# Optimization experiments

Hardware: AMD Instinct MI355X
Metric: run time of the kernel (lower is better)

Reference implementation:

```python
import jax, jax.numpy as jnp
import numpy as np

B, C = 16384, 2048
DELTA_REL = 0.1


def setup_inputs() -> dict:
    key = jax.random.key(0)
    k1, k2, k3 = jax.random.split(key, 3)
    logits = jax.random.normal(k1, (B, C), dtype=jnp.float32)
    u = jax.random.uniform(k2, (B, C), dtype=jnp.float32)
    lab = (jax.random.uniform(k3, (B, C)) > 0.7).astype(jnp.float32)
    targets = jnp.where(u < 0.4, jnp.float32(jnp.nan), lab)
    return {"logits": logits, "targets": targets, "epoch": 3}


def _large_loss_rejection(logits, targets, epoch):
    unknown = jnp.isnan(targets)
    # unknown_to_negative: NaN -> 0 (negative label)
    t = jnp.where(unknown, 0.0, targets)
    # stable BCE-with-logits: softplus(x) - x*t
    losses = jax.nn.softplus(logits) - logits * t

    # --- no-grad mask construction ---
    ul = jax.lax.stop_gradient(losses) * unknown.astype(losses.dtype)
    percent = jnp.minimum(epoch * DELTA_REL, 1.0).astype(jnp.float32)
    n_unknown = jnp.count_nonzero(ul)
    k = jnp.round(n_unknown.astype(jnp.float32) * percent).astype(jnp.int32)
    k = jnp.maximum(k, 1)
    # k-th largest value of flattened unknown losses = topk(k).values.min()
    sorted_desc = jnp.sort(ul.reshape(-1))[::-1]
    loss_threshold = jax.lax.dynamic_slice(sorted_desc, (k - 1,), (1,))[0]
    lambdas = jnp.where(ul > loss_threshold, 0.0, 1.0)

    return losses * lambdas  # reduction='none'


def reference(logits, targets, epoch):
    return _large_loss_rejection(logits, targets, epoch)
```

## Files before the change

kernel.cpp:

```cpp
#include <hip/hip_runtime.h>
#include <math.h>

typedef float    f32x4 __attribute__((ext_vector_type(4)));
typedef unsigned u32x4 __attribute__((ext_vector_type(4)));

#define HBIG_OFF   0u
#define H12_OFF    16384u
#define H64_OFF    20480u
#define SH12_OFF   20544u
#define SHSUB_OFF  24640u
#define CTRL_OFF   24840u
#define FINE_OFF   24864u
#define ZERO_WORDS 25376u
#define GRAY_OFF   25376u
#define GRAY_CAP   440000u
#define EB_OFF     (GRAY_OFF + GRAY_CAP)
#define CAND_OFF   25376u
#define CAND_CAP   880000u
#define LBUF       2048u
#define DELTA_S    2500LL
#define VMARGIN    16384u

#define FLOOR_BITS 0x36000000u


__device__ __forceinline__ float softplus_exact(float x) {
    float ax = fabsf(x);
    float e = (float)exp(-(double)ax);
    float l = (float)log1p((double)e);
    return fmaxf(x, 0.0f) + l;
}
__device__ __forceinline__ unsigned exact_bits(float x) {
    return __float_as_uint(softplus_exact(x));
}

__device__ __forceinline__ unsigned refine_core(float x, float ax, float e,
                                                float sp) {
    unsigned cb = __float_as_uint(sp);
    float mf = 64.0f + 8.0f * ax;
    if (x < 0.0f) mf += __builtin_amdgcn_rcpf(e);
    bool need = (cb < FLOOR_BITS) || (mf >= 524288.0f);
    if (!need) {
        unsigned m = (unsigned)mf;
        unsigned low = cb & 0xFFFFFu;
        need = (low < m) || (low >= 0x100000u - m);
    }
    if (need) cb = exact_bits(x);
    return cb;
}
__device__ __forceinline__ unsigned refine_A(float x) {
    float ax = fabsf(x);
    float e = __expf(-ax);
    float sp = fmaxf(x, 0.0f) + __logf(1.0f + e);
    return refine_core(x, ax, e, sp);
}
__device__ __forceinline__ unsigned known_loss_bits(float x, float t) {
    float ax = fabsf(x);
    float e = __expf(-ax);
    float sp = fmaxf(x, 0.0f) + __logf(1.0f + e);
    return __float_as_uint(sp - x * t);
}

__global__ __launch_bounds__(256) void k0a_shist(
    const float* __restrict__ lg, const float* __restrict__ tg,
    unsigned* __restrict__ ws, long long n) {
    __shared__ unsigned sh[4096];
    for (int i = threadIdx.x; i < 4096; i += 256) sh[i] = 0;
    __syncthreads();
    long long units = n >> 9;
    long long u = (long long)blockIdx.x * 256 + threadIdx.x;
    if (u < units) {
        const f32x4* lg4 = (const f32x4*)lg;
        const f32x4* tg4 = (const f32x4*)tg;
        long long b = u * 128;
        f32x4 xa = lg4[b], xb = lg4[b + 1];
        f32x4 ta = tg4[b], tb = tg4[b + 1];
        float xs[8] = {xa.x, xa.y, xa.z, xa.w, xb.x, xb.y, xb.z, xb.w};
        float ts[8] = {ta.x, ta.y, ta.z, ta.w, tb.x, tb.y, tb.z, tb.w};
#pragma unroll
        for (int c = 0; c < 8; ++c)
            if (isnan(ts[c])) {
                unsigned cb = refine_A(xs[c]);
                if (cb) atomicAdd(&sh[cb >> 20], 1u);
            }
    }
    __syncthreads();
    for (int i = threadIdx.x; i < 4096; i += 256)
        if (sh[i]) atomicAdd(&ws[SH12_OFF + i], sh[i]);
}

__global__ __launch_bounds__(256) void k0b_sbin(
    unsigned* __restrict__ ws, const int* __restrict__ epoch_ptr) {
    const unsigned* sh12 = ws + SH12_OFF;
    unsigned* ctrl = ws + CTRL_OFF;
    __shared__ unsigned long long chunk[256];
    int t = threadIdx.x;
    unsigned long long s = 0;
    for (int j = 0; j < 16; ++j) s += sh12[t * 16 + j];
    chunk[t] = s;
    __syncthreads();
    if (t == 0) {
        unsigned long long tot = 0;
        for (int c = 0; c < 256; ++c) tot += chunk[c];
        if (tot == 0) {
            ctrl[7] = 1u;
            ctrl[8] = 0u; ctrl[9] = 0u; ctrl[19] = 0u;
            ctrl[17] = 0u; ctrl[18] = 0u;
            return;
        }
        int epoch = epoch_ptr[0];
        float percent = fminf((float)epoch * 0.1f, 1.0f);
        long long ks = (long long)((double)percent * (double)tot + 0.5);
        if (ks < 1) ks = 1;
        if (ks > (long long)tot) ks = (long long)tot;
        long long cum = 0;
        int bE = 0;
        for (int c = 255; c >= 0; --c) {
            if (cum + (long long)chunk[c] >= ks) {
                long long cc = cum;
                for (int j = 15; j >= 0; --j) {
                    unsigned v = sh12[c * 16 + j];
                    if (cc + (long long)v >= ks) { bE = c * 16 + j; break; }
                    cc += v;
                }
                break;
            }
            cum += chunk[c];
        }
        ctrl[13] = (unsigned)bE;
        ctrl[17] = (bE > 0) ? (unsigned)(bE - 1) : 0u;
        ctrl[18] = (bE < 4095) ? (unsigned)(bE + 1) : 4095u;
        ctrl[19] = (unsigned)ks;
    }
}

__global__ __launch_bounds__(256) void k0c_ssub(
    const float* __restrict__ lg, const float* __restrict__ tg,
    unsigned* __restrict__ ws, long long n) {
    if (ws[CTRL_OFF + 7] != 0u) return;
    unsigned lob = ws[CTRL_OFF + 17], hib = ws[CTRL_OFF + 18];
    unsigned rlo = lob << 20, rhi = (hib + 1u) << 20;
    __shared__ unsigned sh[192];
    if (threadIdx.x < 192) sh[threadIdx.x] = 0;
    __syncthreads();
    long long units = n >> 9;
    long long u = (long long)blockIdx.x * 256 + threadIdx.x;
    if (u < units) {
        const f32x4* lg4 = (const f32x4*)lg;
        const f32x4* tg4 = (const f32x4*)tg;
        long long b = u * 128;
        f32x4 xa = lg4[b], xb = lg4[b + 1];
        f32x4 ta = tg4[b], tb = tg4[b + 1];
        float xs[8] = {xa.x, xa.y, xa.z, xa.w, xb.x, xb.y, xb.z, xb.w};
        float ts[8] = {ta.x, ta.y, ta.z, ta.w, tb.x, tb.y, tb.z, tb.w};
#pragma unroll
        for (int c = 0; c < 8; ++c)
            if (isnan(ts[c])) {
                unsigned cb = refine_A(xs[c]);
                if (cb >= rlo && cb < rhi && (hib < 4095u || cb >= rlo))
                    atomicAdd(&sh[(cb - rlo) >> 14], 1u);
            }
    }
    __syncthreads();
    if (threadIdx.x < 192 && sh[threadIdx.x])
        atomicAdd(&ws[SHSUB_OFF + threadIdx.x], sh[threadIdx.x]);
}

__global__ __launch_bounds__(256) void k0d_window(unsigned* __restrict__ ws) {
    unsigned* ctrl = ws + CTRL_OFF;
    if (ctrl[7] != 0u) return;
    __shared__ unsigned long long red[256];
    __shared__ unsigned arr[192];
    int t = threadIdx.x;
    unsigned hib = ctrl[18];
    unsigned long long s = 0;
    for (int b = t; b < 4096; b += 256)
        if ((unsigned)b > hib) s += ws[SH12_OFF + b];
    red[t] = s;
    if (t < 192) arr[t] = ws[SHSUB_OFF + t];
    __syncthreads();
    for (int off = 128; off > 0; off >>= 1) {
        if (t < off) red[t] += red[t + off];
        __syncthreads();
    }
    if (t == 0) {
        unsigned lob = ctrl[17];
        unsigned base = lob << 20;
        int nsub = (int)(hib - lob + 1u) * 64;
        long long ks = (long long)ctrl[19];
        long long lo_t = ks - DELTA_S;
        long long hi_t = ks + DELTA_S;
        long long cum = (long long)red[0];
        unsigned est_hi = base + ((unsigned)nsub << 14);
        unsigned est_lo = base;
        bool fh = false, fl = false;
        for (int j = nsub - 1; j >= 0; --j) {
            if (!fh && cum + (long long)arr[j] > lo_t) {
                est_hi = base + ((unsigned)(j + 1) << 14);
                fh = true;
            }
            cum += arr[j];
            if (!fl && cum >= hi_t) {
                est_lo = base + ((unsigned)j << 14);
                fl = true;
            }
            if (fh && fl) break;
        }
        if (!fh) est_hi = base;
        ctrl[8] = est_lo;
        ctrl[9] = est_hi;
    }
}

__device__ __forceinline__ unsigned kA_elem(float x, float t, unsigned idx,
                                            unsigned* __restrict__ shh,
                                            unsigned* __restrict__ sha,
                                            unsigned* __restrict__ buf,
                                            unsigned* __restrict__ lcnt,
                                            unsigned elo, unsigned ehi) {
    float ax = fabsf(x);
    float e = __expf(-ax);
    float sp = fmaxf(x, 0.0f) + __logf(1.0f + e);
    if (isnan(t)) {
        unsigned cb = refine_core(x, ax, e, sp);
        if (cb != 0u) atomicAdd(&shh[cb >> 20], 1u);
        if (cb >= ehi) { atomicAdd(sha, 1u); return 0u; }
        if (cb >= elo) {
            unsigned li = atomicAdd(lcnt, 1u);
            if (li < LBUF) buf[li] = idx;
        }
        return cb;
    }
    return __float_as_uint(sp - x * t);
}

__global__ __launch_bounds__(256) void kA_main(
    const float* __restrict__ lg, const float* __restrict__ tg,
    float* __restrict__ out, unsigned* __restrict__ ws, long long n) {
    __shared__ unsigned shh[4096];
    __shared__ unsigned buf[LBUF];
    __shared__ unsigned lcnt, sha, gbase;
    for (int i = threadIdx.x; i < 4096; i += 256) shh[i] = 0;
    if (threadIdx.x == 0) { lcnt = 0; sha = 0; }
    __syncthreads();
    unsigned elo = ws[CTRL_OFF + 8], ehi = ws[CTRL_OFF + 9];

    long long n8 = n >> 3;
    long long tid = (long long)blockIdx.x * 256 + threadIdx.x;
    long long stride = (long long)gridDim.x * 256;
    const f32x4* lg4 = (const f32x4*)lg;
    const f32x4* tg4 = (const f32x4*)tg;
    f32x4* out4 = (f32x4*)out;

    long long i = tid;
    f32x4 xa, xb, ta, tb;
    if (i < n8) {
        xa = lg4[2 * i]; xb = lg4[2 * i + 1];
        ta = __builtin_nontemporal_load(&tg4[2 * i]);
        tb = __builtin_nontemporal_load(&tg4[2 * i + 1]);
    }
    while (i < n8) {
        long long j = i + stride;
        f32x4 nxa, nxb, nta, ntb;
        if (j < n8) {
            nxa = lg4[2 * j]; nxb = lg4[2 * j + 1];
            nta = __builtin_nontemporal_load(&tg4[2 * j]);
            ntb = __builtin_nontemporal_load(&tg4[2 * j + 1]);
        }
        unsigned base = (unsigned)(i * 8);
        f32x4 oa, ob_;
        oa.x = __uint_as_float(kA_elem(xa.x, ta.x, base + 0, shh, &sha, buf, &lcnt, elo, ehi));
        oa.y = __uint_as_float(kA_elem(xa.y, ta.y, base + 1, shh, &sha, buf, &lcnt, elo, ehi));
        oa.z = __uint_as_float(kA_elem(xa.z, ta.z, base + 2, shh, &sha, buf, &lcnt, elo, ehi));
        oa.w = __uint_as_float(kA_elem(xa.w, ta.w, base + 3, shh, &sha, buf, &lcnt, elo, ehi));
        ob_.x = __uint_as_float(kA_elem(xb.x, tb.x, base + 4, shh, &sha, buf, &lcnt, elo, ehi));
        ob_.y = __uint_as_float(kA_elem(xb.y, tb.y, base + 5, shh, &sha, buf, &lcnt, elo, ehi));
        ob_.z = __uint_as_float(kA_elem(xb.z, tb.z, base + 6, shh, &sha, buf, &lcnt, elo, ehi));
        ob_.w = __uint_as_float(kA_elem(xb.w, tb.w, base + 7, shh, &sha, buf, &lcnt, elo, ehi));
        out4[2 * i] = oa;
        out4[2 * i + 1] = ob_;
        xa = nxa; xb = nxb; ta = nta; tb = ntb;
        i = j;
    }
    if (tid == 0) {
        for (long long q = (n >> 3) << 3; q < n; ++q)
            out[q] = __uint_as_float(
                kA_elem(lg[q], tg[q], (unsigned)q, shh, &sha, buf, &lcnt, elo, ehi));
    }
    __syncthreads();
    for (int q = threadIdx.x; q < 4096; q += 256)
        if (shh[q]) atomicAdd(&ws[H12_OFF + q], shh[q]);
    if (threadIdx.x == 0) {
        if (sha) atomicAdd(&ws[CTRL_OFF + 11], sha);
        unsigned add = (lcnt > LBUF) ? (GRAY_CAP + 1u) : lcnt;
        gbase = atomicAdd(&ws[CTRL_OFF + 10], add);
    }
    __syncthreads();
    unsigned c2 = lcnt < LBUF ? lcnt : LBUF;
    for (unsigned q = threadIdx.x; q < c2; q += 256) {
        unsigned gi = gbase + q;
        if (gi < GRAY_CAP) ws[GRAY_OFF + gi] = buf[q];
    }
}

__global__ __launch_bounds__(256) void k2_route(
    unsigned* __restrict__ ws, const int* __restrict__ epoch_ptr) {
    const unsigned* hist12 = ws + H12_OFF;
    unsigned* ctrl = ws + CTRL_OFF;
    __shared__ unsigned long long chunk[256];
    int t = threadIdx.x;
    unsigned long long s = 0;
    for (int j = 0; j < 16; ++j) s += hist12[t * 16 + j];
    chunk[t] = s;
    __syncthreads();
    if (t == 0) {
        unsigned long long tot = 0;
        for (int c = 0; c < 256; ++c) tot += chunk[c];
        int epoch = epoch_ptr[0];
        float percent = fminf((float)epoch * 0.1f, 1.0f);
        float nf = (float)tot;
        float kr = rintf(nf * percent);
        long long k = (long long)kr;
        if (k < 1) k = 1;
        long long cum = 0;
        int b = -1;
        long long kprime = 0;
        for (int c = 255; c >= 0; --c) {
            if (cum + (long long)chunk[c] >= k) {
                long long cc = cum;
                for (int j = 15; j >= 0; --j) {
                    unsigned v = hist12[c * 16 + j];
                    if (cc + (long long)v >= k) {
                        b = c * 16 + j; kprime = k - cc; break;
                    }
                    cc += v;
                }
                break;
            }
            cum += chunk[c];
        }
        ctrl[0] = (unsigned)b;
        ctrl[1] = (unsigned)kprime;
        if (b < 0) {
            ctrl[2] = 0u;
            ctrl[4] = 0xFFFFFFFFu;
            ctrl[6] = 0u;
            ctrl[7] = 2u;
            return;
        }
        unsigned lo12 = (unsigned)b << 20;
        double vlo = (double)__uint_as_float(lo12);
        double vhi = (double)__uint_as_float(lo12 + 0xFFFFFu);
        double mb = 1e9;
        if (vlo > 1e-30) {
            double xlo = vlo + log1p(-exp(-vlo)) - 0.001;
            double xhi = vhi + log1p(-exp(-vhi)) + 0.001;
            double axmax = fmax(fabs(xlo), fabs(xhi));
            mb = 64.0 + 8.0 * ceil(axmax);
            if (xlo < 0.0) mb += exp(fmin(-xlo, 30.0));
            mb *= 2.0;
        }
        ctrl[6] = (mb >= 8192.0) ? 8192u : (unsigned)mb;
        unsigned f = ctrl[7];
        unsigned g = ctrl[10], a = ctrl[11];
        unsigned elo = ctrl[8], ehi = ctrl[9];
        long long rank = k - (long long)a;
        if (g > GRAY_CAP || rank < 1 || rank > (long long)g ||
            ehi < elo + 2u * VMARGIN)
            f = 1u;
        else {
            ctrl[12] = (unsigned)rank;
            unsigned W = ehi - elo;
            unsigned sft = 0;
            while (((unsigned long long)16384u << sft) < (unsigned long long)W)
                ++sft;
            ctrl[15] = sft;
        }
        ctrl[7] = f;
    }
}

__global__ __launch_bounds__(256) void G1_exact(
    const float* __restrict__ lg, unsigned* __restrict__ ws) {
    if (ws[CTRL_OFF + 7] != 0u) return;
    unsigned gcount = ws[CTRL_OFF + 10];
    unsigned elo = ws[CTRL_OFF + 8], ehi = ws[CTRL_OFF + 9];
    unsigned sft = ws[CTRL_OFF + 15];
    long long tid = (long long)blockIdx.x * 256 + threadIdx.x;
    long long stride = (long long)gridDim.x * 256;
    for (long long g = tid; g < (long long)gcount; g += stride) {
        unsigned idx = ws[GRAY_OFF + g];
        unsigned eb = exact_bits(lg[idx]);
        ws[EB_OFF + g] = eb;
        unsigned bin = (eb < elo) ? 0u
                     : (eb >= ehi) ? 16383u : ((eb - elo) >> sft);
        if (bin > 16383u) bin = 16383u;
        atomicAdd(&ws[HBIG_OFF + bin], 1u);
    }
}

__global__ __launch_bounds__(1024) void G2a_selbin(unsigned* __restrict__ ws) {
    unsigned* ctrl = ws + CTRL_OFF;
    if (ctrl[7] != 0u) return;
    __shared__ unsigned long long csum[1024];
    int t = threadIdx.x;
    unsigned long long s = 0;
    for (int j = 0; j < 16; ++j) s += ws[HBIG_OFF + t * 16 + j];
    csum[t] = s;
    __syncthreads();
    if (t == 0) {
        long long rank = (long long)ctrl[12];
        long long cum = 0;
        int sel = -1;
        long long rem = 1;
        for (int c = 1023; c >= 0; --c) {
            if (cum + (long long)csum[c] >= rank) {
                long long cc = cum;
                for (int j = 15; j >= 0; --j) {
                    unsigned v = ws[HBIG_OFF + c * 16 + j];
                    if (cc + (long long)v >= rank) {
                        sel = c * 16 + j; rem = rank - cc; break;
                    }
                    cc += v;
                }
                break;
            }
            cum += csum[c];
        }
        if (sel < 0) { ctrl[7] = 1u; return; }
        ctrl[14] = (unsigned)sel;
        ctrl[16] = (unsigned)rem;
    }
}

__global__ __launch_bounds__(256) void G2b_fine(unsigned* __restrict__ ws) {
    if (ws[CTRL_OFF + 7] != 0u) return;
    unsigned gcount = ws[CTRL_OFF + 10];
    unsigned elo = ws[CTRL_OFF + 8], ehi = ws[CTRL_OFF + 9];
    unsigned sft = ws[CTRL_OFF + 15];
    unsigned bsel = ws[CTRL_OFF + 14];
    long long tid = (long long)blockIdx.x * 256 + threadIdx.x;
    long long stride = (long long)gridDim.x * 256;
    for (long long g = tid; g < (long long)gcount; g += stride) {
        unsigned eb = ws[EB_OFF + g];
        if (eb >= elo && eb < ehi) {
            unsigned off = eb - elo;
            if ((off >> sft) == bsel)
                atomicAdd(&ws[FINE_OFF + (off - (bsel << sft))], 1u);
        }
    }
}

__global__ __launch_bounds__(512) void G2c_thr(unsigned* __restrict__ ws) {
    unsigned* ctrl = ws + CTRL_OFF;
    if (ctrl[7] != 0u) return;
    __shared__ unsigned fine[512];
    int t = threadIdx.x;
    unsigned sft = ctrl[15];
    unsigned binw = 1u << sft;
    if (binw > 512u) { if (t == 0) ctrl[7] = 1u; return; }
    if ((unsigned)t < binw) fine[t] = ws[FINE_OFF + t];
    __syncthreads();
    if (t == 0) {
        unsigned elo = ctrl[8], ehi = ctrl[9];
        unsigned binlo = elo + (ctrl[14] << sft);
        long long rem = (long long)ctrl[16];
        long long cum = 0;
        bool found = false;
        unsigned thr = 0;
        for (int o = (int)binw - 1; o >= 0; --o) {
            cum += fine[o];
            if (cum >= rem) { thr = binlo + (unsigned)o; found = true; break; }
        }
        if (!found || thr < elo + VMARGIN || thr > ehi - VMARGIN)
            ctrl[7] = 1u;
        else
            ctrl[2] = thr;
    }
}

__global__ __launch_bounds__(256) void kD_fix(
    unsigned* __restrict__ ob, const unsigned* __restrict__ ws) {
    if (ws[CTRL_OFF + 7] != 0u) return;
    unsigned gcount = ws[CTRL_OFF + 10];
    unsigned thr = ws[CTRL_OFF + 2];
    long long tid = (long long)blockIdx.x * 256 + threadIdx.x;
    long long stride = (long long)gridDim.x * 256;
    for (long long g = tid; g < (long long)gcount; g += stride) {
        if (ws[EB_OFF + g] > thr) ob[ws[GRAY_OFF + g]] = 0u;
    }
}

__global__ __launch_bounds__(256) void fkB(
    const float* __restrict__ lg, const float* __restrict__ tg,
    unsigned* __restrict__ ws, long long n) {
    if (ws[CTRL_OFF + 7] != 1u) return;
    unsigned b12 = ws[CTRL_OFF + 0];
    if (b12 == 0xFFFFFFFFu) return;
    unsigned lo12 = b12 << 20, hi12 = lo12 + (1u << 20);
    unsigned m = ws[CTRL_OFF + 6];
    __shared__ unsigned sh[64];
    __shared__ float buf[LBUF];
    __shared__ unsigned lcnt, gbase;
    if (threadIdx.x < 64) sh[threadIdx.x] = 0;
    if (threadIdx.x == 0) lcnt = 0;
    __syncthreads();
    float* cand = (float*)(ws + CAND_OFF);
    unsigned* cnt = ws + CTRL_OFF + 3;
    long long n4 = n >> 2;
    long long tid = (long long)blockIdx.x * 256 + threadIdx.x;
    long long stride = (long long)gridDim.x * 256;
    const f32x4* lg4 = (const f32x4*)lg;
    const f32x4* tg4 = (const f32x4*)tg;
    for (long long i = tid; i < n4; i += stride) {
        f32x4 x4 = lg4[i], t4 = tg4[i];
        float xs[4] = {x4.x, x4.y, x4.z, x4.w};
        float ts[4] = {t4.x, t4.y, t4.z, t4.w};
#pragma unroll
        for (int c = 0; c < 4; ++c) {
            if (isnan(ts[c])) {
                float x = xs[c];
                unsigned cb = refine_A(x);
                if (cb >= lo12 && cb < hi12) {
                    unsigned d = cb & 16383u;
                    unsigned rB = (d < m || d >= 16384u - m) ? exact_bits(x) : cb;
                    atomicAdd(&sh[(rB >> 14) & 63u], 1u);
                    unsigned li = atomicAdd(&lcnt, 1u);
                    if (li < LBUF) buf[li] = x;
                }
            }
        }
    }
    if (tid == 0) {
        for (long long q = (n4 << 2); q < n; ++q) {
            if (isnan(tg[q])) {
                float x = lg[q];
                unsigned cb = refine_A(x);
                if (cb >= lo12 && cb < hi12) {
                    unsigned d = cb & 16383u;
                    unsigned rB = (d < m || d >= 16384u - m) ? exact_bits(x) : cb;
                    atomicAdd(&sh[(rB >> 14) & 63u], 1u);
                    unsigned idx = atomicAdd(cnt, 1u);
                    if (idx < CAND_CAP) cand[idx] = x;
                }
            }
        }
    }
    __syncthreads();
    if (threadIdx.x < 64 && sh[threadIdx.x])
        atomicAdd(&ws[H64_OFF + threadIdx.x], sh[threadIdx.x]);
    if (threadIdx.x == 0) {
        unsigned add = (lcnt > LBUF) ? (CAND_CAP + 1u) : lcnt;
        gbase = atomicAdd(cnt, add);
    }
    __syncthreads();
    unsigned c2 = lcnt < LBUF ? lcnt : LBUF;
    for (unsigned q = threadIdx.x; q < c2; q += 256) {
        unsigned gi = gbase + q;
        if (gi < CAND_CAP) cand[gi] = buf[q];
    }
}

__global__ void fk4(unsigned* __restrict__ ws) {
    unsigned* ctrl = ws + CTRL_OFF;
    if (ctrl[7] != 1u) return;
    if (ctrl[0] == 0xFFFFFFFFu) return;
    if (threadIdx.x == 0) {
        long long kprime = (long long)ctrl[1];
        long long cum = 0;
        int s = 0;
        long long kpp = 1;
        for (int j = 63; j >= 0; --j) {
            unsigned v = ws[H64_OFF + j];
            if (cum + (long long)v >= kprime) { s = j; kpp = kprime - cum; break; }
            cum += v;
        }
        ctrl[4] = (ctrl[0] << 20) + ((unsigned)s << 14);
        ctrl[5] = (unsigned)kpp;
    }
}

__global__ __launch_bounds__(256) void fkC(
    const float* __restrict__ lg, const float* __restrict__ tg,
    unsigned* __restrict__ ws, long long n) {
    if (ws[CTRL_OFF + 7] != 1u) return;
    unsigned wlo = ws[CTRL_OFF + 4];
    if (wlo == 0xFFFFFFFFu) return;
    unsigned whi = wlo + 16384u;
    unsigned m = ws[CTRL_OFF + 6];
    unsigned b12 = ws[CTRL_OFF + 0];
    unsigned lo12 = b12 << 20, hi12 = lo12 + (1u << 20);
    unsigned glo = (wlo - lo12 > m) ? wlo - m : lo12;
    unsigned ghi = (hi12 - whi > m) ? whi + m : hi12;
    unsigned count = ws[CTRL_OFF + 3];
    long long tid = (long long)blockIdx.x * 256 + threadIdx.x;
    long long stride = (long long)gridDim.x * 256;
    if (count <= CAND_CAP) {
        const float* cand = (const float*)(ws + CAND_OFF);
        for (long long i = tid; i < (long long)count; i += stride) {
            float x = cand[i];
            unsigned u = refine_A(x);
            if (u >= glo && u < ghi) {
                unsigned eb = exact_bits(x);
                unsigned d = u & 16383u;
                unsigned rB = (d < m || d >= 16384u - m) ? eb : u;
                if (rB >= wlo && rB < whi) {
                    unsigned off = eb - wlo;
                    if (off < 16384u) atomicAdd(&ws[HBIG_OFF + off], 1u);
                }
            }
        }
    } else {
        for (long long q = tid; q < n; q += stride) {
            if (isnan(tg[q])) {
                float x = lg[q];
                unsigned u = refine_A(x);
                if (u >= glo && u < ghi) {
                    unsigned eb = exact_bits(x);
                    unsigned d = u & 16383u;
                    unsigned rB = (d < m || d >= 16384u - m) ? eb : u;
                    if (rB >= wlo && rB < whi) {
                        unsigned off = eb - wlo;
                        if (off < 16384u) atomicAdd(&ws[HBIG_OFF + off], 1u);
                    }
                }
            }
        }
    }
}

__global__ __launch_bounds__(1024) void fk6(unsigned* __restrict__ ws) {
    unsigned* ctrl = ws + CTRL_OFF;
    if (ctrl[7] != 1u) return;
    if (ctrl[4] == 0xFFFFFFFFu) return;
    __shared__ unsigned long long csum[1024];
    int t = threadIdx.x;
    unsigned long long s = 0;
    for (int j = 0; j < 16; ++j) s += ws[HBIG_OFF + t * 16 + j];
    csum[t] = s;
    __syncthreads();
    if (t == 0) {
        long long kpp = (long long)ctrl[5];
        long long cum = 0;
        int sel = 0;
        long long rem = kpp;
        for (int c = 1023; c >= 0; --c) {
            if (cum + (long long)csum[c] >= kpp) { sel = c; rem = kpp - cum; break; }
            cum += csum[c];
        }
        long long cc = 0;
        int bsel = 0;
        for (int j = 15; j >= 0; --j) {
            unsigned v = ws[HBIG_OFF + sel * 16 + j];
            if (cc + (long long)v >= rem) { bsel = j; break; }
            cc += v;
        }
        ctrl[2] = ctrl[4] + (unsigned)(sel * 16 + bsel);
    }
}

__global__ __launch_bounds__(256) void fkD(
    const float* __restrict__ lg, const float* __restrict__ tg,
    float* __restrict__ out, const unsigned* __restrict__ ws, long long n) {
    if (ws[CTRL_OFF + 7] != 1u) return;
    unsigned thr = ws[CTRL_OFF + 2];
    unsigned m = ws[CTRL_OFF + 6];
    long long n4 = n >> 2;
    long long tid = (long long)blockIdx.x * 256 + threadIdx.x;
    long long stride = (long long)gridDim.x * 256;
    const f32x4* lg4 = (const f32x4*)lg;
    const f32x4* tg4 = (const f32x4*)tg;
    f32x4* out4 = (f32x4*)out;
    for (long long i = tid; i < n4; i += stride) {
        f32x4 x4 = lg4[i], t4 = tg4[i];
        float xs[4] = {x4.x, x4.y, x4.z, x4.w};
        float ts[4] = {t4.x, t4.y, t4.z, t4.w};
        f32x4 o;
        float os[4];
#pragma unroll
        for (int c = 0; c < 4; ++c) {
            float x = xs[c], t = ts[c];
            if (isnan(t)) {
                unsigned cb = refine_A(x);
                unsigned udiff = (cb > thr) ? cb - thr : thr - cb;
                unsigned r;
                if (udiff <= m) {
                    unsigned eb = exact_bits(x);
                    r = (eb > thr) ? 0u : eb;
                } else {
                    r = (cb > thr) ? 0u : cb;
                }
                os[c] = __uint_as_float(r);
            } else {
                os[c] = __uint_as_float(known_loss_bits(x, t));
            }
        }
        o.x = os[0]; o.y = os[1]; o.z = os[2]; o.w = os[3];
        out4[i] = o;
    }
    if (tid == 0) {
        for (long long q = (n4 << 2); q < n; ++q) {
            float x = lg[q], t = tg[q];
            if (isnan(t)) {
                unsigned cb = refine_A(x);
                unsigned udiff = (cb > thr) ? cb - thr : thr - cb;
                unsigned eb, r;
                if (udiff <= m) { eb = exact_bits(x); r = (eb > thr) ? 0u : eb; }
                else r = (cb > thr) ? 0u : cb;
                out[q] = __uint_as_float(r);
            } else {
                out[q] = __uint_as_float(known_loss_bits(x, t));
            }
        }
    }
}

extern "C" void kernel_launch(void* const* d_in, const int* in_sizes, int n_in,
                              void* d_out, int out_size, void* d_ws, size_t ws_size,
                              hipStream_t stream) {
    const float* lg = (const float*)d_in[0];
    const float* tg = (const float*)d_in[1];
    const int* epoch = (const int*)d_in[2];
    float* out = (float*)d_out;
    unsigned* ob = (unsigned*)d_out;
    unsigned* ws = (unsigned*)d_ws;
    long long n = (long long)in_sizes[0];

    (void)hipMemsetAsync(d_ws, 0, (size_t)ZERO_WORDS * 4, stream);

    k0a_shist<<<256, 256, 0, stream>>>(lg, tg, ws, n);
    k0b_sbin<<<1, 256, 0, stream>>>(ws, epoch);
    k0c_ssub<<<256, 256, 0, stream>>>(lg, tg, ws, n);
    k0d_window<<<1, 256, 0, stream>>>(ws);
    kA_main<<<2048, 256, 0, stream>>>(lg, tg, out, ws, n);
    k2_route<<<1, 256, 0, stream>>>(ws, epoch);
    G1_exact<<<128, 256, 0, stream>>>(lg, ws);
    G2a_selbin<<<1, 1024, 0, stream>>>(ws);
    G2b_fine<<<128, 256, 0, stream>>>(ws);
    G2c_thr<<<1, 512, 0, stream>>>(ws);
    kD_fix<<<128, 256, 0, stream>>>(ob, ws);
    fkB<<<2048, 256, 0, stream>>>(lg, tg, ws, n);
    fk4<<<1, 64, 0, stream>>>(ws);
    fkC<<<1024, 256, 0, stream>>>(lg, tg, ws, n);
    fk6<<<1, 1024, 0, stream>>>(ws);
    fkD<<<2048, 256, 0, stream>>>(lg, tg, out, ws, n);
}
```

Measured before the change: 266.7 us.

## Drop per-element histogram in main pass, stash gray-zone logits, defer histogram to fallback

```diff
diff --git a/kernel.cpp b/kernel.cpp
--- a/kernel.cpp
+++ b/kernel.cpp
@@ -13,7 +13,7 @@
 #define FINE_OFF   24864u
 #define ZERO_WORDS 25376u
 #define GRAY_OFF   25376u
-#define GRAY_CAP   440000u
+#define GRAY_CAP   450000u
 #define EB_OFF     (GRAY_OFF + GRAY_CAP)
 #define CAND_OFF   25376u
 #define CAND_CAP   880000u
@@ -213,21 +213,21 @@
 }
 
 __device__ __forceinline__ unsigned kA_elem(float x, float t, unsigned idx,
-                                            unsigned* __restrict__ shh,
-                                            unsigned* __restrict__ sha,
-                                            unsigned* __restrict__ buf,
-                                            unsigned* __restrict__ lcnt,
-                                            unsigned elo, unsigned ehi) {
+                                            unsigned elo, unsigned ehi,
+                                            unsigned& nz, unsigned& ab,
+                                            unsigned* __restrict__ bufi,
+                                            unsigned* __restrict__ bufx,
+                                            unsigned* __restrict__ lcnt) {
     float ax = fabsf(x);
     float e = __expf(-ax);
     float sp = fmaxf(x, 0.0f) + __logf(1.0f + e);
     if (isnan(t)) {
         unsigned cb = refine_core(x, ax, e, sp);
-        if (cb != 0u) atomicAdd(&shh[cb >> 20], 1u);
-        if (cb >= ehi) { atomicAdd(sha, 1u); return 0u; }
+        nz += (cb != 0u) ? 1u : 0u;
+        if (cb >= ehi) { ++ab; return 0u; }
         if (cb >= elo) {
             unsigned li = atomicAdd(lcnt, 1u);
-            if (li < LBUF) buf[li] = idx;
+            if (li < LBUF) { bufi[li] = idx; bufx[li] = __float_as_uint(x); }
         }
         return cb;
     }
@@ -237,13 +237,15 @@
 __global__ __launch_bounds__(256) void kA_main(
     const float* __restrict__ lg, const float* __restrict__ tg,
     float* __restrict__ out, unsigned* __restrict__ ws, long long n) {
-    __shared__ unsigned shh[4096];
-    __shared__ unsigned buf[LBUF];
-    __shared__ unsigned lcnt, sha, gbase;
-    for (int i = threadIdx.x; i < 4096; i += 256) shh[i] = 0;
-    if (threadIdx.x == 0) { lcnt = 0; sha = 0; }
-    __syncthreads();
+    __shared__ unsigned bufi[LBUF];
+    __shared__ unsigned bufx[LBUF];
+    __shared__ unsigned lcnt, gbase, snz, sab;
+    if (threadIdx.x == 0) { lcnt = 0; snz = 0; sab = 0; }
+    __syncthreads();
+    unsigned flag = ws[CTRL_OFF + 7];
     unsigned elo = ws[CTRL_OFF + 8], ehi = ws[CTRL_OFF + 9];
+    if (flag != 0u) { elo = 0xFFFFFFFFu; ehi = 0xFFFFFFFFu; }
+    unsigned nz = 0, ab = 0;
 
     long long n8 = n >> 3;
     long long tid = (long long)blockIdx.x * 256 + threadIdx.x;
@@ -252,46 +254,74 @@
     const f32x4* tg4 = (const f32x4*)tg;
     f32x4* out4 = (f32x4*)out;
 
-    long long i = tid;
-    f32x4 xa, xb, ta, tb;
-    if (i < n8) {
-        xa = lg4[2 * i]; xb = lg4[2 * i + 1];
-        ta = __builtin_nontemporal_load(&tg4[2 * i]);
-        tb = __builtin_nontemporal_load(&tg4[2 * i + 1]);
-    }
-    while (i < n8) {
-        long long j = i + stride;
-        f32x4 nxa, nxb, nta, ntb;
-        if (j < n8) {
-            nxa = lg4[2 * j]; nxb = lg4[2 * j + 1];
-            nta = __builtin_nontemporal_load(&tg4[2 * j]);
-            ntb = __builtin_nontemporal_load(&tg4[2 * j + 1]);
-        }
-        unsigned base = (unsigned)(i * 8);
-        f32x4 oa, ob_;
-        oa.x = __uint_as_float(kA_elem(xa.x, ta.x, base + 0, shh, &sha, buf, &lcnt, elo, ehi));
-        oa.y = __uint_as_float(kA_elem(xa.y, ta.y, base + 1, shh, &sha, buf, &lcnt, elo, ehi));
-        oa.z = __uint_as_float(kA_elem(xa.z, ta.z, base + 2, shh, &sha, buf, &lcnt, elo, ehi));
-        oa.w = __uint_as_float(kA_elem(xa.w, ta.w, base + 3, shh, &sha, buf, &lcnt, elo, ehi));
-        ob_.x = __uint_as_float(kA_elem(xb.x, tb.x, base + 4, shh, &sha, buf, &lcnt, elo, ehi));
-        ob_.y = __uint_as_float(kA_elem(xb.y, tb.y, base + 5, shh, &sha, buf, &lcnt, elo, ehi));
-        ob_.z = __uint_as_float(kA_elem(xb.z, tb.z, base + 6, shh, &sha, buf, &lcnt, elo, ehi));
-        ob_.w = __uint_as_float(kA_elem(xb.w, tb.w, base + 7, shh, &sha, buf, &lcnt, elo, ehi));
-        out4[2 * i] = oa;
-        out4[2 * i + 1] = ob_;
-        xa = nxa; xb = nxb; ta = nta; tb = ntb;
-        i = j;
+    if (n8 % stride == 0) {
+        long long iters = n8 / stride;
+        f32x4 xa0, xb0, ta0, tb0, xa1, xb1, ta1, tb1;
+        {
+            long long i = tid;
+            xa0 = lg4[2 * i]; xb0 = lg4[2 * i + 1];
+            ta0 = __builtin_nontemporal_load(&tg4[2 * i]);
+            tb0 = __builtin_nontemporal_load(&tg4[2 * i + 1]);
+        }
+        if (iters > 1) {
+            long long i = tid + stride;
+            xa1 = lg4[2 * i]; xb1 = lg4[2 * i + 1];
+            ta1 = __builtin_nontemporal_load(&tg4[2 * i]);
+            tb1 = __builtin_nontemporal_load(&tg4[2 * i + 1]);
+        }
+        for (long long it = 0; it < iters; ++it) {
+            f32x4 pa, pb, pta, ptb;
+            if (it + 2 < iters) {
+                long long i = tid + (it + 2) * stride;
+                pa = lg4[2 * i]; pb = lg4[2 * i + 1];
+                pta = __builtin_nontemporal_load(&tg4[2 * i]);
+                ptb = __builtin_nontemporal_load(&tg4[2 * i + 1]);
+            }
+            long long i = tid + it * stride;
+            unsigned base = (unsigned)(i * 8);
+            f32x4 oa, ob_;
+            oa.x = __uint_as_float(kA_elem(xa0.x, ta0.x, base + 0, elo, ehi, nz, ab, bufi, bufx, &lcnt));
+            oa.y = __uint_as_float(kA_elem(xa0.y, ta0.y, base + 1, elo, ehi, nz, ab, bufi, bufx, &lcnt));
+            oa.z = __uint_as_float(kA_elem(xa0.z, ta0.z, base + 2, elo, ehi, nz, ab, bufi, bufx, &lcnt));
+            oa.w = __uint_as_float(kA_elem(xa0.w, ta0.w, base + 3, elo, ehi, nz, ab, bufi, bufx, &lcnt));
+            ob_.x = __uint_as_float(kA_elem(xb0.x, tb0.x, base + 4, elo, ehi, nz, ab, bufi, bufx, &lcnt));
+            ob_.y = __uint_as_float(kA_elem(xb0.y, tb0.y, base + 5, elo, ehi, nz, ab, bufi, bufx, &lcnt));
+            ob_.z = __uint_as_float(kA_elem(xb0.z, tb0.z, base + 6, elo, ehi, nz, ab, bufi, bufx, &lcnt));
+            ob_.w = __uint_as_float(kA_elem(xb0.w, tb0.w, base + 7, elo, ehi, nz, ab, bufi, bufx, &lcnt));
+            out4[2 * i] = oa;
+            out4[2 * i + 1] = ob_;
+            xa0 = xa1; xb0 = xb1; ta0 = ta1; tb0 = tb1;
+            xa1 = pa; xb1 = pb; ta1 = pta; tb1 = ptb;
+        }
+    } else {
+        for (long long i = tid; i < n8; i += stride) {
+            f32x4 xa = lg4[2 * i], xb = lg4[2 * i + 1];
+            f32x4 ta = tg4[2 * i], tb = tg4[2 * i + 1];
+            unsigned base = (unsigned)(i * 8);
+            f32x4 oa, ob_;
+            oa.x = __uint_as_float(kA_elem(xa.x, ta.x, base + 0, elo, ehi, nz, ab, bufi, bufx, &lcnt));
+            oa.y = __uint_as_float(kA_elem(xa.y, ta.y, base + 1, elo, ehi, nz, ab, bufi, bufx, &lcnt));
+            oa.z = __uint_as_float(kA_elem(xa.z, ta.z, base + 2, elo, ehi, nz, ab, bufi, bufx, &lcnt));
+            oa.w = __uint_as_float(kA_elem(xa.w, ta.w, base + 3, elo, ehi, nz, ab, bufi, bufx, &lcnt));
+            ob_.x = __uint_as_float(kA_elem(xb.x, tb.x, base + 4, elo, ehi, nz, ab, bufi, bufx, &lcnt));
+            ob_.y = __uint_as_float(kA_elem(xb.y, tb.y, base + 5, elo, ehi, nz, ab, bufi, bufx, &lcnt));
+            ob_.z = __uint_as_float(kA_elem(xb.z, tb.z, base + 6, elo, ehi, nz, ab, bufi, bufx, &lcnt));
+            ob_.w = __uint_as_float(kA_elem(xb.w, tb.w, base + 7, elo, ehi, nz, ab, bufi, bufx, &lcnt));
+            out4[2 * i] = oa;
+            out4[2 * i + 1] = ob_;
+        }
     }
     if (tid == 0) {
         for (long long q = (n >> 3) << 3; q < n; ++q)
             out[q] = __uint_as_float(
-                kA_elem(lg[q], tg[q], (unsigned)q, shh, &sha, buf, &lcnt, elo, ehi));
-    }
-    __syncthreads();
-    for (int q = threadIdx.x; q < 4096; q += 256)
-        if (shh[q]) atomicAdd(&ws[H12_OFF + q], shh[q]);
+                kA_elem(lg[q], tg[q], (unsigned)q, elo, ehi, nz, ab, bufi, bufx, &lcnt));
+    }
+    if (nz) atomicAdd(&snz, nz);
+    if (ab) atomicAdd(&sab, ab);
+    __syncthreads();
     if (threadIdx.x == 0) {
-        if (sha) atomicAdd(&ws[CTRL_OFF + 11], sha);
+        if (snz) atomicAdd(&ws[CTRL_OFF + 20], snz);
+        if (sab) atomicAdd(&ws[CTRL_OFF + 11], sab);
         unsigned add = (lcnt > LBUF) ? (GRAY_CAP + 1u) : lcnt;
         gbase = atomicAdd(&ws[CTRL_OFF + 10], add);
     }
@@ -299,14 +329,192 @@
     unsigned c2 = lcnt < LBUF ? lcnt : LBUF;
     for (unsigned q = threadIdx.x; q < c2; q += 256) {
         unsigned gi = gbase + q;
-        if (gi < GRAY_CAP) ws[GRAY_OFF + gi] = buf[q];
-    }
-}
-
-__global__ __launch_bounds__(256) void k2_route(
+        if (gi < GRAY_CAP) {
+            ws[GRAY_OFF + gi] = bufi[q];
+            ws[EB_OFF + gi] = bufx[q];
+        }
+    }
+}
+
+__global__ void k2_route(unsigned* __restrict__ ws,
+                         const int* __restrict__ epoch_ptr) {
+    if (threadIdx.x != 0) return;
+    unsigned* ctrl = ws + CTRL_OFF;
+    unsigned tot = ctrl[20];
+    int epoch = epoch_ptr[0];
+    float percent = fminf((float)epoch * 0.1f, 1.0f);
+    float nf = (float)tot;
+    float kr = rintf(nf * percent);
+    long long k = (long long)kr;
+    if (k < 1) k = 1;
+    if (tot == 0u) { ctrl[2] = 0u; ctrl[7] = 2u; return; }
+    if (ctrl[7] != 0u) return;
+    unsigned g = ctrl[10], a = ctrl[11];
+    unsigned elo = ctrl[8], ehi = ctrl[9];
+    long long rank = k - (long long)a;
+    if (g > GRAY_CAP || rank < 1 || rank > (long long)g ||
+        ehi < elo + 2u * VMARGIN) {
+        ctrl[7] = 1u;
+        return;
+    }
+    ctrl[12] = (unsigned)rank;
+    unsigned W = ehi - elo;
+    unsigned sft = 0;
+    while (((unsigned long long)16384u << sft) < (unsigned long long)W) ++sft;
+    ctrl[15] = sft;
+}
+
+__global__ __launch_bounds__(256) void G1_exact(unsigned* __restrict__ ws) {
+    if (ws[CTRL_OFF + 7] != 0u) return;
+    unsigned gcount = ws[CTRL_OFF + 10];
+    unsigned elo = ws[CTRL_OFF + 8], ehi = ws[CTRL_OFF + 9];
+    unsigned sft = ws[CTRL_OFF + 15];
+    long long tid = (long long)blockIdx.x * 256 + threadIdx.x;
+    long long stride = (long long)gridDim.x * 256;
+    for (long long g = tid; g < (long long)gcount; g += stride) {
+        float x = __uint_as_float(ws[EB_OFF + g]);
+        unsigned eb = exact_bits(x);
+        ws[EB_OFF + g] = eb;
+        unsigned bin = (eb < elo) ? 0u
+                     : (eb >= ehi) ? 16383u : ((eb - elo) >> sft);
+        if (bin > 16383u) bin = 16383u;
+        atomicAdd(&ws[HBIG_OFF + bin], 1u);
+    }
+}
+
+__global__ __launch_bounds__(1024) void G2a_selbin(unsigned* __restrict__ ws) {
+    unsigned* ctrl = ws + CTRL_OFF;
+    if (ctrl[7] != 0u) return;
+    __shared__ unsigned long long csum[1024];
+    int t = threadIdx.x;
+    unsigned long long s = 0;
+    for (int j = 0; j < 16; ++j) s += ws[HBIG_OFF + t * 16 + j];
+    csum[t] = s;
+    __syncthreads();
+    if (t == 0) {
+        long long rank = (long long)ctrl[12];
+        long long cum = 0;
+        int sel = -1;
+        long long rem = 1;
+        for (int c = 1023; c >= 0; --c) {
+            if (cum + (long long)csum[c] >= rank) {
+                long long cc = cum;
+                for (int j = 15; j >= 0; --j) {
+                    unsigned v = ws[HBIG_OFF + c * 16 + j];
+                    if (cc + (long long)v >= rank) {
+                        sel = c * 16 + j; rem = rank - cc; break;
+                    }
+                    cc += v;
+                }
+                break;
+            }
+            cum += csum[c];
+        }
+        if (sel < 0) { ctrl[7] = 1u; return; }
+        ctrl[14] = (unsigned)sel;
+        ctrl[16] = (unsigned)rem;
+    }
+}
+
+__global__ __launch_bounds__(256) void G2b_fine(unsigned* __restrict__ ws) {
+    if (ws[CTRL_OFF + 7] != 0u) return;
+    unsigned gcount = ws[CTRL_OFF + 10];
+    unsigned elo = ws[CTRL_OFF + 8], ehi = ws[CTRL_OFF + 9];
+    unsigned sft = ws[CTRL_OFF + 15];
+    unsigned bsel = ws[CTRL_OFF + 14];
+    long long tid = (long long)blockIdx.x * 256 + threadIdx.x;
+    long long stride = (long long)gridDim.x * 256;
+    for (long long g = tid; g < (long long)gcount; g += stride) {
+        unsigned eb = ws[EB_OFF + g];
+        if (eb >= elo && eb < ehi) {
+            unsigned off = eb - elo;
+            if ((off >> sft) == bsel)
+                atomicAdd(&ws[FINE_OFF + (off - (bsel << sft))], 1u);
+        }
+    }
+}
+
+__global__ __launch_bounds__(512) void G2c_thr(unsigned* __restrict__ ws) {
+    unsigned* ctrl = ws + CTRL_OFF;
+    if (ctrl[7] != 0u) return;
+    __shared__ unsigned fine[512];
+    int t = threadIdx.x;
+    unsigned sft = ctrl[15];
+    unsigned binw = 1u << sft;
+    if (binw > 512u) { if (t == 0) ctrl[7] = 1u; return; }
+    if ((unsigned)t < binw) fine[t] = ws[FINE_OFF + t];
+    __syncthreads();
+    if (t == 0) {
+        unsigned elo = ctrl[8], ehi = ctrl[9];
+        unsigned binlo = elo + (ctrl[14] << sft);
+        long long rem = (long long)ctrl[16];
+        long long cum = 0;
+        bool found = false;
+        unsigned thr = 0;
+        for (int o = (int)binw - 1; o >= 0; --o) {
+            cum += fine[o];
+            if (cum >= rem) { thr = binlo + (unsigned)o; found = true; break; }
+        }
+        if (!found || thr < elo + VMARGIN || thr > ehi - VMARGIN)
+            ctrl[7] = 1u;
+        else
+            ctrl[2] = thr;
+    }
+}
+
+__global__ __launch_bounds__(256) void kD_fix(
+    unsigned* __restrict__ ob, const unsigned* __restrict__ ws) {
+    if (ws[CTRL_OFF + 7] != 0u) return;
+    unsigned gcount = ws[CTRL_OFF + 10];
+    unsigned thr = ws[CTRL_OFF + 2];
+    long long tid = (long long)blockIdx.x * 256 + threadIdx.x;
+    long long stride = (long long)gridDim.x * 256;
+    for (long long g = tid; g < (long long)gcount; g += stride) {
+        if (ws[EB_OFF + g] > thr) ob[ws[GRAY_OFF + g]] = 0u;
+    }
+}
+
+__global__ __launch_bounds__(256) void fkA_hist(
+    const float* __restrict__ lg, const float* __restrict__ tg,
+    unsigned* __restrict__ ws, long long n) {
+    if (ws[CTRL_OFF + 7] != 1u) return;
+    __shared__ unsigned sh[4096];
+    for (int i = threadIdx.x; i < 4096; i += 256) sh[i] = 0;
+    __syncthreads();
+    long long n4 = n >> 2;
+    long long tid = (long long)blockIdx.x * 256 + threadIdx.x;
+    long long stride = (long long)gridDim.x * 256;
+    const f32x4* lg4 = (const f32x4*)lg;
+    const f32x4* tg4 = (const f32x4*)tg;
+    for (long long i = tid; i < n4; i += stride) {
+        f32x4 x4 = lg4[i], t4 = tg4[i];
+        float xs[4] = {x4.x, x4.y, x4.z, x4.w};
+        float ts[4] = {t4.x, t4.y, t4.z, t4.w};
+#pragma unroll
+        for (int c = 0; c < 4; ++c)
+            if (isnan(ts[c])) {
+                unsigned cb = refine_A(xs[c]);
+                if (cb) atomicAdd(&sh[cb >> 20], 1u);
+            }
+    }
+    if (tid == 0) {
+        for (long long q = (n4 << 2); q < n; ++q)
+            if (isnan(tg[q])) {
+                unsigned cb = refine_A(lg[q]);
+                if (cb) atomicAdd(&sh[cb >> 20], 1u);
+            }
+    }
+    __syncthreads();
+    for (int i = threadIdx.x; i < 4096; i += 256)
+        if (sh[i]) atomicAdd(&ws[H12_OFF + i], sh[i]);
+}
+
+__global__ __launch_bounds__(256) void fk2_sel(
     unsigned* __restrict__ ws, const int* __restrict__ epoch_ptr) {
+    unsigned* ctrl = ws + CTRL_OFF;
+    if (ctrl[7] != 1u) return;
+    for (unsigned i = threadIdx.x; i < 16384u; i += 256) ws[HBIG_OFF + i] = 0;
     const unsigned* hist12 = ws + H12_OFF;
-    unsigned* ctrl = ws + CTRL_OFF;
     __shared__ unsigned long long chunk[256];
     int t = threadIdx.x;
     unsigned long long s = 0;
@@ -316,6 +524,7 @@
     if (t == 0) {
         unsigned long long tot = 0;
         for (int c = 0; c < 256; ++c) tot += chunk[c];
+        if (tot == 0) { ctrl[2] = 0u; ctrl[7] = 2u; return; }
         int epoch = epoch_ptr[0];
         float percent = fminf((float)epoch * 0.1f, 1.0f);
         float nf = (float)tot;
@@ -341,13 +550,6 @@
         }
         ctrl[0] = (unsigned)b;
         ctrl[1] = (unsigned)kprime;
-        if (b < 0) {
-            ctrl[2] = 0u;
-            ctrl[4] = 0xFFFFFFFFu;
-            ctrl[6] = 0u;
-            ctrl[7] = 2u;
-            return;
-        }
         unsigned lo12 = (unsigned)b << 20;
         double vlo = (double)__uint_as_float(lo12);
         double vhi = (double)__uint_as_float(lo12 + 0xFFFFFu);
@@ -361,133 +563,6 @@
             mb *= 2.0;
         }
         ctrl[6] = (mb >= 8192.0) ? 8192u : (unsigned)mb;
-        unsigned f = ctrl[7];
-        unsigned g = ctrl[10], a = ctrl[11];
-        unsigned elo = ctrl[8], ehi = ctrl[9];
-        long long rank = k - (long long)a;
-        if (g > GRAY_CAP || rank < 1 || rank > (long long)g ||
-            ehi < elo + 2u * VMARGIN)
-            f = 1u;
-        else {
-            ctrl[12] = (unsigned)rank;
-            unsigned W = ehi - elo;
-            unsigned sft = 0;
-            while (((unsigned long long)16384u << sft) < (unsigned long long)W)
-                ++sft;
-            ctrl[15] = sft;
-        }
-        ctrl[7] = f;
-    }
-}
-
-__global__ __launch_bounds__(256) void G1_exact(
-    const float* __restrict__ lg, unsigned* __restrict__ ws) {
-    if (ws[CTRL_OFF + 7] != 0u) return;
-    unsigned gcount = ws[CTRL_OFF + 10];
-    unsigned elo = ws[CTRL_OFF + 8], ehi = ws[CTRL_OFF + 9];
-    unsigned sft = ws[CTRL_OFF + 15];
-    long long tid = (long long)blockIdx.x * 256 + threadIdx.x;
-    long long stride = (long long)gridDim.x * 256;
-    for (long long g = tid; g < (long long)gcount; g += stride) {
-        unsigned idx = ws[GRAY_OFF + g];
-        unsigned eb = exact_bits(lg[idx]);
-        ws[EB_OFF + g] = eb;
-        unsigned bin = (eb < elo) ? 0u
-                     : (eb >= ehi) ? 16383u : ((eb - elo) >> sft);
-        if (bin > 16383u) bin = 16383u;
-        atomicAdd(&ws[HBIG_OFF + bin], 1u);
-    }
-}
-
-__global__ __launch_bounds__(1024) void G2a_selbin(unsigned* __restrict__ ws) {
-    unsigned* ctrl = ws + CTRL_OFF;
-    if (ctrl[7] != 0u) return;
-    __shared__ unsigned long long csum[1024];
-    int t = threadIdx.x;
-    unsigned long long s = 0;
-    for (int j = 0; j < 16; ++j) s += ws[HBIG_OFF + t * 16 + j];
-    csum[t] = s;
-    __syncthreads();
-    if (t == 0) {
-        long long rank = (long long)ctrl[12];
-        long long cum = 0;
-        int sel = -1;
-        long long rem = 1;
-        for (int c = 1023; c >= 0; --c) {
-            if (cum + (long long)csum[c] >= rank) {
-                long long cc = cum;
-                for (int j = 15; j >= 0; --j) {
-                    unsigned v = ws[HBIG_OFF + c * 16 + j];
-                    if (cc + (long long)v >= rank) {
-                        sel = c * 16 + j; rem = rank - cc; break;
-                    }
-                    cc += v;
-                }
-                break;
-            }
-            cum += csum[c];
-        }
-        if (sel < 0) { ctrl[7] = 1u; return; }
-        ctrl[14] = (unsigned)sel;
-        ctrl[16] = (unsigned)rem;
-    }
-}
-
-__global__ __launch_bounds__(256) void G2b_fine(unsigned* __restrict__ ws) {
-    if (ws[CTRL_OFF + 7] != 0u) return;
-    unsigned gcount = ws[CTRL_OFF + 10];
-    unsigned elo = ws[CTRL_OFF + 8], ehi = ws[CTRL_OFF + 9];
-    unsigned sft = ws[CTRL_OFF + 15];
-    unsigned bsel = ws[CTRL_OFF + 14];
-    long long tid = (long long)blockIdx.x * 256 + threadIdx.x;
-    long long stride = (long long)gridDim.x * 256;
-    for (long long g = tid; g < (long long)gcount; g += stride) {
-        unsigned eb = ws[EB_OFF + g];
-        if (eb >= elo && eb < ehi) {
-            unsigned off = eb - elo;
-            if ((off >> sft) == bsel)
-                atomicAdd(&ws[FINE_OFF + (off - (bsel << sft))], 1u);
-        }
-    }
-}
-
-__global__ __launch_bounds__(512) void G2c_thr(unsigned* __restrict__ ws) {
-    unsigned* ctrl = ws + CTRL_OFF;
-    if (ctrl[7] != 0u) return;
-    __shared__ unsigned fine[512];
-    int t = threadIdx.x;
-    unsigned sft = ctrl[15];
-    unsigned binw = 1u << sft;
-    if (binw > 512u) { if (t == 0) ctrl[7] = 1u; return; }
-    if ((unsigned)t < binw) fine[t] = ws[FINE_OFF + t];
-    __syncthreads();
-    if (t == 0) {
-        unsigned elo = ctrl[8], ehi = ctrl[9];
-        unsigned binlo = elo + (ctrl[14] << sft);
-        long long rem = (long long)ctrl[16];
-        long long cum = 0;
-        bool found = false;
-        unsigned thr = 0;
-        for (int o = (int)binw - 1; o >= 0; --o) {
-            cum += fine[o];
-            if (cum >= rem) { thr = binlo + (unsigned)o; found = true; break; }
-        }
-        if (!found || thr < elo + VMARGIN || thr > ehi - VMARGIN)
-            ctrl[7] = 1u;
-        else
-            ctrl[2] = thr;
-    }
-}
-
-__global__ __launch_bounds__(256) void kD_fix(
-    unsigned* __restrict__ ob, const unsigned* __restrict__ ws) {
-    if (ws[CTRL_OFF + 7] != 0u) return;
-    unsigned gcount = ws[CTRL_OFF + 10];
-    unsigned thr = ws[CTRL_OFF + 2];
-    long long tid = (long long)blockIdx.x * 256 + threadIdx.x;
-    long long stride = (long long)gridDim.x * 256;
-    for (long long g = tid; g < (long long)gcount; g += stride) {
-        if (ws[EB_OFF + g] > thr) ob[ws[GRAY_OFF + g]] = 0u;
     }
 }
 
@@ -496,7 +571,6 @@
     unsigned* __restrict__ ws, long long n) {
     if (ws[CTRL_OFF + 7] != 1u) return;
     unsigned b12 = ws[CTRL_OFF + 0];
-    if (b12 == 0xFFFFFFFFu) return;
     unsigned lo12 = b12 << 20, hi12 = lo12 + (1u << 20);
     unsigned m = ws[CTRL_OFF + 6];
     __shared__ unsigned sh[64];
@@ -564,7 +638,6 @@
 __global__ void fk4(unsigned* __restrict__ ws) {
     unsigned* ctrl = ws + CTRL_OFF;
     if (ctrl[7] != 1u) return;
-    if (ctrl[0] == 0xFFFFFFFFu) return;
     if (threadIdx.x == 0) {
         long long kprime = (long long)ctrl[1];
         long long cum = 0;
@@ -585,7 +658,6 @@
     unsigned* __restrict__ ws, long long n) {
     if (ws[CTRL_OFF + 7] != 1u) return;
     unsigned wlo = ws[CTRL_OFF + 4];
-    if (wlo == 0xFFFFFFFFu) return;
     unsigned whi = wlo + 16384u;
     unsigned m = ws[CTRL_OFF + 6];
     unsigned b12 = ws[CTRL_OFF + 0];
@@ -632,7 +704,6 @@
 __global__ __launch_bounds__(1024) void fk6(unsigned* __restrict__ ws) {
     unsigned* ctrl = ws + CTRL_OFF;
     if (ctrl[7] != 1u) return;
-    if (ctrl[4] == 0xFFFFFFFFu) return;
     __shared__ unsigned long long csum[1024];
     int t = threadIdx.x;
     unsigned long long s = 0;
@@ -733,15 +804,17 @@
     k0c_ssub<<<256, 256, 0, stream>>>(lg, tg, ws, n);
     k0d_window<<<1, 256, 0, stream>>>(ws);
     kA_main<<<2048, 256, 0, stream>>>(lg, tg, out, ws, n);
-    k2_route<<<1, 256, 0, stream>>>(ws, epoch);
-    G1_exact<<<128, 256, 0, stream>>>(lg, ws);
+    k2_route<<<1, 64, 0, stream>>>(ws, epoch);
+    G1_exact<<<128, 256, 0, stream>>>(ws);
     G2a_selbin<<<1, 1024, 0, stream>>>(ws);
     G2b_fine<<<128, 256, 0, stream>>>(ws);
     G2c_thr<<<1, 512, 0, stream>>>(ws);
     kD_fix<<<128, 256, 0, stream>>>(ob, ws);
-    fkB<<<2048, 256, 0, stream>>>(lg, tg, ws, n);
+    fkA_hist<<<1024, 256, 0, stream>>>(lg, tg, ws, n);
+    fk2_sel<<<1, 256, 0, stream>>>(ws, epoch);
+    fkB<<<1024, 256, 0, stream>>>(lg, tg, ws, n);
     fk4<<<1, 64, 0, stream>>>(ws);
-    fkC<<<1024, 256, 0, stream>>>(lg, tg, ws, n);
+    fkC<<<512, 256, 0, stream>>>(lg, tg, ws, n);
     fk6<<<1, 1024, 0, stream>>>(ws);
     fkD<<<2048, 256, 0, stream>>>(lg, tg, out, ws, n);
 }
```

Result: slower. 279.8 us (+4.9%).
